# Kernel optimization log

Hardware: AMD Instinct MI355X
Metric: run time of the kernel (lower is better)

The kernel has to match this reference:

```python
import jax, jax.numpy as jnp
import numpy as np

L_MAX = 3


def setup_inputs() -> dict:
    key = jax.random.key(0)
    k1, k2, k3, k4 = jax.random.split(key, 4)
    B, V, P, Cin, R, Cout = 8, 4096, 32, 64, 2, 128
    N = (L_MAX + 1) ** 2  # 16 spherical-harmonic coeffs
    signal = jax.random.normal(k1, (B, V, Cin), dtype=jnp.float32)
    # gather_nd indices: [..., 0] = batch index, [..., 1] = point index
    bidx = jnp.broadcast_to(jnp.arange(B, dtype=jnp.int32)[:, None, None], (B, V, P))
    pidx = jax.random.randint(k2, (B, V, P), 0, V, dtype=jnp.int32)
    patches_idx = jnp.stack([bidx, pidx], axis=-1)
    conv_kernel = jax.random.normal(k3, (B, V, P, R, N), dtype=jnp.float32)
    kernel_weights = jax.random.normal(k4, (Cout, Cin, R, L_MAX + 1), dtype=jnp.float32)
    biases = jnp.zeros((Cout,), dtype=jnp.float32)
    return {"signal": signal, "patches_idx": patches_idx, "conv_kernel": conv_kernel,
            "kernel_weights": kernel_weights, "biases": biases}


def reference(signal, patches_idx, conv_kernel, kernel_weights, biases):
    l_max = kernel_weights.shape[-1] - 1
    # gather neighbor patches: [B, V, P, Cin]
    patches = signal[patches_idx[..., 0], patches_idx[..., 1]]
    # per-point conv over patch dim: [B, V, Cin, R, N]
    y = jnp.einsum('bvprn,bvpc->bvcrn', conv_kernel, patches)
    y = y * y
    # SH-invariant power per degree l: sum over the 2l+1 orders m
    blocks = []
    p = 0
    for l in range(l_max + 1):
        blocks.append(jnp.sum(y[..., p:p + 2 * l + 1], axis=-1))
        p += 2 * l + 1
    y = jnp.stack(blocks, axis=-1)  # [B, V, Cin, R, l_max+1]
    y = jnp.sqrt(jnp.maximum(y, 1e-4))
    out = jnp.einsum('ijrn,bvjrn->bvi', kernel_weights, y) + biases
    return jax.nn.relu(out)
```

## Files before the change

### kernel.cpp

```cpp
#include <hip/hip_runtime.h>
#include <cstddef>

namespace {

constexpr int kV = 4096;
constexpr int kBlocks = 8 * kV / 16;

typedef float f32x16 __attribute__((ext_vector_type(16)));
typedef float f32x4  __attribute__((ext_vector_type(4)));
typedef short bf16x8 __attribute__((ext_vector_type(8)));

union U8 { unsigned u[4]; uint4 q; bf16x8 v; };

__device__ inline unsigned pk_bf16(float a, float b) {
    unsigned ua = __float_as_uint(a);
    unsigned ub = __float_as_uint(b);
    ua = (ua + 0x7FFFu + ((ua >> 16) & 1u)) >> 16;
    ub = (ub + 0x7FFFu + ((ub >> 16) & 1u)) & 0xFFFF0000u;
    return ua | ub;
}

__device__ inline unsigned cvt_pk(float a, float b) {
    unsigned r;
    asm("v_cvt_pk_bf16_f32 %0, %1, %2" : "=v"(r) : "v"(a), "v"(b));
    return r;
}

__device__ inline float fsqrt(float x) {
    float r;
    asm("v_sqrt_f32 %0, %1" : "=v"(r) : "v"(x));
    return r;
}

__global__ void convW(const float* __restrict__ W, unsigned* __restrict__ Wb) {
    const int i = blockIdx.x * 256 + threadIdx.x;
    const float2 w2 = ((const float2*)W)[i];
    Wb[i] = pk_bf16(w2.x, w2.y);
}

__global__ __launch_bounds__(256, 2)
void fused(const float* __restrict__ signal,
           const int* __restrict__ pidx_g,
           const float* __restrict__ ck_g,
           const unsigned short* __restrict__ Wb,
           const float* __restrict__ bias,
           float* __restrict__ out)
{
    __shared__ __align__(16) unsigned short zbf[16][520];

    const int t = threadIdx.x;

    const int b      = blockIdx.x & 7;
    const int v_base = ((blockIdx.x >> 3) & 255) * 16;

    const int w    = t >> 6;
    const int lane = t & 63;
    const int n31  = lane & 31;
    const int h    = lane >> 5;

    const float* sgb = signal + (size_t)b * kV * 64;

    int vsl[4];
    #pragma unroll
    for (int vg = 0; vg < 4; ++vg)
        vsl[vg] = pidx_g[((((size_t)b * kV + v_base + vg * 4 + w) * 32) + n31) * 2 + 1];

    float sP[32];
    float cP[2][16];

    auto prefetch_sig = [&](int vg) {
        #pragma unroll
        for (int pp = 0; pp < 16; ++pp) {
            const int vs0 = __builtin_amdgcn_readlane(vsl[vg], 2 * pp);
            const int vs1 = __builtin_amdgcn_readlane(vsl[vg], 2 * pp + 1);
            sP[2 * pp    ] = sgb[(size_t)vs0 * 64 + lane];
            sP[2 * pp + 1] = sgb[(size_t)vs1 * 64 + lane];
        }
    };
    auto prefetch_ck = [&](int vg, int buf) {
        const size_t bv = (size_t)b * kV + (v_base + vg * 4 + w);
        const float* ckv = ck_g + bv * 1024;
        #pragma unroll
        for (int j2 = 0; j2 < 4; ++j2) {
            const int p0 = 8 * h + 2 * j2;
            cP[buf][4 * j2 + 0] = __builtin_nontemporal_load(&ckv[(p0     ) * 32 + n31]);
            cP[buf][4 * j2 + 1] = __builtin_nontemporal_load(&ckv[(p0 +  1) * 32 + n31]);
            cP[buf][4 * j2 + 2] = __builtin_nontemporal_load(&ckv[(p0 + 16) * 32 + n31]);
            cP[buf][4 * j2 + 3] = __builtin_nontemporal_load(&ckv[(p0 + 17) * 32 + n31]);
        }
    };

    prefetch_ck(0, 0);
    prefetch_sig(0);
    prefetch_ck(1, 1);

    #pragma unroll
    for (int vg = 0; vg < 4; ++vg) {
        const int g = vg * 4 + w;
        const int cur = vg & 1;

        U8 A0, A1;
        #pragma unroll
        for (int j2 = 0; j2 < 4; ++j2) {
            A0.u[j2] = cvt_pk(cP[cur][4 * j2 + 0], cP[cur][4 * j2 + 1]);
            A1.u[j2] = cvt_pk(cP[cur][4 * j2 + 2], cP[cur][4 * j2 + 3]);
        }

        unsigned pkv[16];
        #pragma unroll
        for (int pp = 0; pp < 16; ++pp)
            pkv[pp] = cvt_pk(sP[2 * pp], sP[2 * pp + 1]);

        U8 B00, B01, B10, B11;
        #pragma unroll
        for (int j2 = 0; j2 < 4; ++j2) {
            auto r0 = __builtin_amdgcn_permlane32_swap(pkv[j2], pkv[4 + j2], false, false);
            B00.u[j2] = r0[0];
            B01.u[j2] = r0[1];
            auto r1 = __builtin_amdgcn_permlane32_swap(pkv[8 + j2], pkv[12 + j2], false, false);
            B10.u[j2] = r1[0];
            B11.u[j2] = r1[1];
        }

        if (vg < 3) prefetch_sig(vg + 1);
        if (vg < 2) prefetch_ck(vg + 2, cur);

        f32x16 acc0, acc1;
        #pragma unroll
        for (int j = 0; j < 16; ++j) { acc0[j] = 0.f; acc1[j] = 0.f; }
        acc0 = __builtin_amdgcn_mfma_f32_32x32x16_bf16(A0.v, B00.v, acc0, 0, 0, 0);
        acc1 = __builtin_amdgcn_mfma_f32_32x32x16_bf16(A0.v, B01.v, acc1, 0, 0, 0);
        acc0 = __builtin_amdgcn_mfma_f32_32x32x16_bf16(A1.v, B10.v, acc0, 0, 0, 0);
        acc1 = __builtin_amdgcn_mfma_f32_32x32x16_bf16(A1.v, B11.v, acc1, 0, 0, 0);

        #pragma unroll
        for (int ct = 0; ct < 2; ++ct) {
            const f32x16 a = ct ? acc1 : acc0;
            float s[16];
            #pragma unroll
            for (int j = 0; j < 16; ++j) s[j] = a[j] * a[j];
            const float o00 = s[0], o10 = s[1] + s[2] + s[3];
            const float o20 = s[4], o30 = s[5] + s[6] + s[7];
            const float o01 = s[8], o11 = s[9] + s[10] + s[11];
            const float o21 = s[12], o31 = s[13] + s[14] + s[15];
            const float x0 = s[0] + s[1] + s[2] + s[3];
            const float x1 = s[4] + s[5] + s[6] + s[7];
            const float x2 = s[8] + s[9] + s[10] + s[11];
            const float x3 = s[12] + s[13] + s[14] + s[15];
            const float e0 = __shfl_xor(h ? x0 : o20, 32);
            const float e1 = __shfl_xor(h ? x1 : o30, 32);
            const float e2 = __shfl_xor(h ? x2 : o21, 32);
            const float e3 = __shfl_xor(h ? x3 : o31, 32);
            if (h == 0) {
                const float z00 = fsqrt(fmaxf(o00,      1e-4f));
                const float z10 = fsqrt(fmaxf(o10,      1e-4f));
                const float z20 = fsqrt(fmaxf(o20 + e0, 1e-4f));
                const float z30 = fsqrt(fmaxf(o30 + e1, 1e-4f));
                const float z01 = fsqrt(fmaxf(o01,      1e-4f));
                const float z11 = fsqrt(fmaxf(o11,      1e-4f));
                const float z21 = fsqrt(fmaxf(o21 + e2, 1e-4f));
                const float z31 = fsqrt(fmaxf(o31 + e3, 1e-4f));
                uint4 d;
                d.x = cvt_pk(z00, z10);
                d.y = cvt_pk(z20, z30);
                d.z = cvt_pk(z01, z11);
                d.w = cvt_pk(z21, z31);
                *(uint4*)&zbf[g][(n31 + 32 * ct) * 8] = d;
            }
        }
    }
    __syncthreads();

    const int m15 = lane & 15;
    const int q   = lane >> 4;
    f32x4 pa0, pa1;
    #pragma unroll
    for (int j = 0; j < 4; ++j) { pa0[j] = 0.f; pa1[j] = 0.f; }
    const int i0 = w * 32 + m15;
    const int i1 = w * 32 + 16 + m15;
    #pragma unroll 4
    for (int ks = 0; ks < 16; ++ks) {
        U8 Az, Bw0, Bw1;
        Az.q  = *(const uint4*)&zbf[m15][ks * 32 + q * 8];
        Bw0.q = *(const uint4*)&Wb[(size_t)i0 * 512 + ks * 32 + q * 8];
        Bw1.q = *(const uint4*)&Wb[(size_t)i1 * 512 + ks * 32 + q * 8];
        pa0 = __builtin_amdgcn_mfma_f32_16x16x32_bf16(Az.v, Bw0.v, pa0, 0, 0, 0);
        pa1 = __builtin_amdgcn_mfma_f32_16x16x32_bf16(Az.v, Bw1.v, pa1, 0, 0, 0);
    }
    const float bi0 = bias[i0], bi1 = bias[i1];
    #pragma unroll
    for (int reg = 0; reg < 4; ++reg) {
        const int g = q * 4 + reg;
        const size_t row = ((size_t)b * kV + v_base + g) * 128;
        __builtin_nontemporal_store(fmaxf(pa0[reg] + bi0, 0.f), &out[row + i0]);
        __builtin_nontemporal_store(fmaxf(pa1[reg] + bi1, 0.f), &out[row + i1]);
    }
}

}

extern "C" void kernel_launch(void* const* d_in, const int* in_sizes, int n_in,
                              void* d_out, int out_size, void* d_ws, size_t ws_size,
                              hipStream_t stream) {
    const float* signal = (const float*)d_in[0];
    const int*   pidx   = (const int*)d_in[1];
    const float* ck     = (const float*)d_in[2];
    const float* W      = (const float*)d_in[3];
    const float* bias   = (const float*)d_in[4];
    float* out = (float*)d_out;
    unsigned* Wb = (unsigned*)d_ws;

    convW<<<dim3(128), dim3(256), 0, stream>>>(W, Wb);
    fused<<<dim3(kBlocks), dim3(256), 0, stream>>>(
        signal, pidx, ck, (const unsigned short*)Wb, bias, out);
}
```

Before: 241.0 us.

## Deepen conv-kernel prefetch to triple buffer and preload W before barrier

The conv_kernel register prefetch moves from double to triple buffering, so three vertex groups of loads are in flight ahead of the MFMA work. In the output GEMM, the first four K-slices of the bf16 weights are loaded before the __syncthreads, and later slices are software-pipelined four steps ahead. Together these aim to hide global-memory latency behind the barrier and the MFMAs. The cost is more VGPRs, which could spill or hurt occupancy under launch_bounds(256,2).

```diff
diff --git a/kernel.cpp b/kernel.cpp
--- a/kernel.cpp
+++ b/kernel.cpp
@@ -66,7 +66,7 @@
         vsl[vg] = pidx_g[((((size_t)b * kV + v_base + vg * 4 + w) * 32) + n31) * 2 + 1];
 
     float sP[32];
-    float cP[2][16];
+    float cP[3][16];
 
     auto prefetch_sig = [&](int vg) {
         #pragma unroll
@@ -91,19 +91,20 @@
     };
 
     prefetch_ck(0, 0);
+    prefetch_ck(1, 1);
     prefetch_sig(0);
-    prefetch_ck(1, 1);
+    prefetch_ck(2, 2);
 
     #pragma unroll
     for (int vg = 0; vg < 4; ++vg) {
-        const int g = vg * 4 + w;
-        const int cur = vg & 1;
+        const int g  = vg * 4 + w;
+        const int cb = vg % 3;
 
         U8 A0, A1;
         #pragma unroll
         for (int j2 = 0; j2 < 4; ++j2) {
-            A0.u[j2] = cvt_pk(cP[cur][4 * j2 + 0], cP[cur][4 * j2 + 1]);
-            A1.u[j2] = cvt_pk(cP[cur][4 * j2 + 2], cP[cur][4 * j2 + 3]);
+            A0.u[j2] = cvt_pk(cP[cb][4 * j2 + 0], cP[cb][4 * j2 + 1]);
+            A1.u[j2] = cvt_pk(cP[cb][4 * j2 + 2], cP[cb][4 * j2 + 3]);
         }
 
         unsigned pkv[16];
@@ -123,7 +124,7 @@
         }
 
         if (vg < 3) prefetch_sig(vg + 1);
-        if (vg < 2) prefetch_ck(vg + 2, cur);
+        if (vg < 1) prefetch_ck(vg + 3, (vg + 3) % 3);
 
         f32x16 acc0, acc1;
         #pragma unroll
@@ -169,25 +170,37 @@
             }
         }
     }
-    __syncthreads();
 
     const int m15 = lane & 15;
     const int q   = lane >> 4;
-    f32x4 pa0, pa1;
-    #pragma unroll
-    for (int j = 0; j < 4; ++j) { pa0[j] = 0.f; pa1[j] = 0.f; }
     const int i0 = w * 32 + m15;
     const int i1 = w * 32 + 16 + m15;
-    #pragma unroll 4
+
+    U8 BwA[4], BwB[4];
+    #pragma unroll
+    for (int j = 0; j < 4; ++j) {
+        BwA[j].q = *(const uint4*)&Wb[(size_t)i0 * 512 + j * 32 + q * 8];
+        BwB[j].q = *(const uint4*)&Wb[(size_t)i1 * 512 + j * 32 + q * 8];
+    }
+    const float bi0 = bias[i0], bi1 = bias[i1];
+
+    __syncthreads();
+
+    f32x4 pa0, pa1;
+    #pragma unroll
+    for (int j = 0; j < 4; ++j) { pa0[j] = 0.f; pa1[j] = 0.f; }
+    #pragma unroll
     for (int ks = 0; ks < 16; ++ks) {
-        U8 Az, Bw0, Bw1;
-        Az.q  = *(const uint4*)&zbf[m15][ks * 32 + q * 8];
-        Bw0.q = *(const uint4*)&Wb[(size_t)i0 * 512 + ks * 32 + q * 8];
-        Bw1.q = *(const uint4*)&Wb[(size_t)i1 * 512 + ks * 32 + q * 8];
-        pa0 = __builtin_amdgcn_mfma_f32_16x16x32_bf16(Az.v, Bw0.v, pa0, 0, 0, 0);
-        pa1 = __builtin_amdgcn_mfma_f32_16x16x32_bf16(Az.v, Bw1.v, pa1, 0, 0, 0);
-    }
-    const float bi0 = bias[i0], bi1 = bias[i1];
+        U8 Az;
+        Az.q = *(const uint4*)&zbf[m15][ks * 32 + q * 8];
+        const U8 b0 = BwA[ks & 3], b1 = BwB[ks & 3];
+        if (ks < 12) {
+            BwA[ks & 3].q = *(const uint4*)&Wb[(size_t)i0 * 512 + (ks + 4) * 32 + q * 8];
+            BwB[ks & 3].q = *(const uint4*)&Wb[(size_t)i1 * 512 + (ks + 4) * 32 + q * 8];
+        }
+        pa0 = __builtin_amdgcn_mfma_f32_16x16x32_bf16(Az.v, b0.v, pa0, 0, 0, 0);
+        pa1 = __builtin_amdgcn_mfma_f32_16x16x32_bf16(Az.v, b1.v, pa1, 0, 0, 0);
+    }
     #pragma unroll
     for (int reg = 0; reg < 4; ++reg) {
         const int g = q * 4 + reg;
```

New measurement: 240.7 us. No clear change (-0.1%).
